# Performance work log

Measured on AMD Instinct MI355X. Metric: run time of the kernel, lower is better.

The kernel has to match this reference:

```python
import jax, jax.numpy as jnp
import numpy as np


def floor_ste(x):
    # forward: floor(x); backward: identity (straight-through estimator)
    return x + jax.lax.stop_gradient(jnp.floor(x) - x)


def _int_polynomial(x_int, sf):
    c0, c1, c2 = 0.35815147, 0.96963238, 1.0
    b_int = floor_ste((c1 / c0) / sf)
    c_int = floor_ste((c2 / c0) / (sf * sf))
    z = x_int * (x_int + b_int) + c_int
    return z, c0 * sf * sf


def _int_exp(x_int, sf):
    x0 = -0.69314718
    n = 15
    x0_int = floor_ste(x0 / sf)
    x_int = jnp.maximum(x_int, n * x0_int)
    q = floor_ste(x_int / x0_int)
    r = x_int - x0_int * q
    exp_int, exp_sf = _int_polynomial(r, sf)
    exp_int = jnp.maximum(floor_ste(exp_int * jnp.exp2(n - q)), 0.0)
    return exp_int, exp_sf / (2.0 ** n)


def _int_softmax(x, sf):
    x_int = x / sf
    x_int = x_int - jnp.max(x_int, axis=-1, keepdims=True)
    exp_int, exp_sf = _int_exp(x_int, sf)
    exp_int_sum = jnp.sum(exp_int, axis=-1, keepdims=True)
    return exp_int, exp_int_sum, exp_sf


def setup_inputs() -> dict:
    key = jax.random.key(0)
    k1, = jax.random.split(key, 1)
    x = jax.random.normal(k1, (2, 16, 1024, 1024), dtype=jnp.float32)
    scale = jnp.float32(0.05)          # activation quantization step
    threshold = jnp.array([0.1], dtype=jnp.float32)  # nn.Parameter init
    return {"x": x, "scale": scale, "threshold": threshold}


def reference(x, scale, threshold):
    output_bit = 8
    threshold_bits = 8
    exp_int, exp_int_sum, exp_sf = _int_softmax(x, scale)
    factor = floor_ste((2.0 ** 32) / exp_int_sum)
    out_scale_A = threshold / (2.0 ** output_bit - 1.0)   # shape [1]
    out_scale_B = 1.0 / (2.0 ** output_bit - 1.0)
    approx_threshold = (floor_ste(threshold * 2.0 ** threshold_bits)
                        * exp_int_sum / (2.0 ** threshold_bits))
    mask_A = exp_int <= approx_threshold
    exp_int_A = jnp.where(mask_A, exp_int, 0.0)
    exp_int_B = jnp.where(mask_A, 0.0, exp_int)
    softmax_int_A = floor_ste(exp_int_A * factor / ((2.0 ** 32) * out_scale_A))
    softmax_int_B = floor_ste(exp_int_B * factor / ((2.0 ** 32) * out_scale_B))
    softmax_int_B = jnp.minimum(softmax_int_B, 255.0)
    return softmax_int_A * out_scale_A + softmax_int_B * out_scale_B
```

## Files before the change

kernel.cpp:

```cpp
#include <hip/hip_runtime.h>
#include <math.h>

#pragma clang fp contract(off)

#define TPB 256
#define ROWLEN 1024

typedef float f32x4 __attribute__((ext_vector_type(4)));

__device__ __forceinline__ float wave_max_dpp(float m) {
    const int NEG_INF = 0xff800000;
    int v;
    v = __builtin_amdgcn_update_dpp(NEG_INF, __float_as_int(m), 0x111, 0xf, 0xf, false);
    m = fmaxf(m, __int_as_float(v));
    v = __builtin_amdgcn_update_dpp(NEG_INF, __float_as_int(m), 0x112, 0xf, 0xf, false);
    m = fmaxf(m, __int_as_float(v));
    v = __builtin_amdgcn_update_dpp(NEG_INF, __float_as_int(m), 0x114, 0xf, 0xf, false);
    m = fmaxf(m, __int_as_float(v));
    v = __builtin_amdgcn_update_dpp(NEG_INF, __float_as_int(m), 0x118, 0xf, 0xf, false);
    m = fmaxf(m, __int_as_float(v));
    v = __builtin_amdgcn_update_dpp(NEG_INF, __float_as_int(m), 0x142, 0xa, 0xf, false);
    m = fmaxf(m, __int_as_float(v));
    v = __builtin_amdgcn_update_dpp(NEG_INF, __float_as_int(m), 0x143, 0xc, 0xf, false);
    m = fmaxf(m, __int_as_float(v));
    return __int_as_float(__builtin_amdgcn_readlane(__float_as_int(m), 63));
}

__device__ __forceinline__ unsigned wave_sum_dpp_u32(unsigned a) {
    int v;
    v = __builtin_amdgcn_update_dpp(0, (int)a, 0x111, 0xf, 0xf, false); a += (unsigned)v;
    v = __builtin_amdgcn_update_dpp(0, (int)a, 0x112, 0xf, 0xf, false); a += (unsigned)v;
    v = __builtin_amdgcn_update_dpp(0, (int)a, 0x114, 0xf, 0xf, false); a += (unsigned)v;
    v = __builtin_amdgcn_update_dpp(0, (int)a, 0x118, 0xf, 0xf, false); a += (unsigned)v;
    v = __builtin_amdgcn_update_dpp(0, (int)a, 0x142, 0xa, 0xf, false); a += (unsigned)v;
    v = __builtin_amdgcn_update_dpp(0, (int)a, 0x143, 0xc, 0xf, false); a += (unsigned)v;
    return (unsigned)__builtin_amdgcn_readlane((int)a, 63);
}

__global__ __launch_bounds__(TPB) void qsplit_int_softmax_kernel(
    const float* __restrict__ x,
    const float* __restrict__ scale_p,
    const float* __restrict__ thr_p,
    float* __restrict__ out)
{
    const int tid  = threadIdx.x;
    const int lane = tid & 63;
    const int wid  = tid >> 6;
    const size_t base = (size_t)blockIdx.x * ROWLEN + (size_t)tid * 4;

    __shared__ float  smax[4];
    __shared__ double ssum[4];

    const float sf  = scale_p[0];
    const float thr = thr_p[0];

    const float rh = 1.0f / sf;
    const float er = __builtin_fmaf(-sf, rh, 1.0f);
    const float rl = rh * er;

    #define DF_DIV(a) ({ float _p = (a) * rh; \
                         float _e = __builtin_fmaf((a), rh, -_p); \
                         _p + __builtin_fmaf((a), rl, _e); })
    const float x0f    = floorf(DF_DIV(-0.69314718f));
    const float bfc    = floorf(DF_DIV(2.7073824f));
    const float s2     = sf * sf;
    const float r2h    = 1.0f / s2;
    const float r2e    = __builtin_fmaf(-s2, r2h, 1.0f);
    const float r2l    = r2h * r2e;
    const float cq     = __builtin_fmaf(2.7921141f, r2l,
                         2.7921141f * r2h);
    const float cfc    = floorf(cq);
    const float clampf = 15.0f * x0f;
    const float invx0f = 1.0f / x0f;

    const float osA  = thr / 255.0f;
    const float osB  = 1.0f / 255.0f;
    const float invA = 1.0f / (4294967296.0f * osA);
    const float invB = 1.0f / (4294967296.0f * osB);
    const float thrq = floorf(thr * 256.0f);

    const f32x4 xv = *(const f32x4*)(x + base);

    float xi[4];
    #pragma unroll
    for (int j = 0; j < 4; ++j) {
        const float xx = xv[j];
        const float p  = xx * rh;
        const float e  = __builtin_fmaf(xx, rh, -p);
        xi[j] = p + __builtin_fmaf(xx, rl, e);
    }

    float m = fmaxf(fmaxf(xi[0], xi[1]), fmaxf(xi[2], xi[3]));
    m = wave_max_dpp(m);
    if (lane == 0) smax[wid] = m;
    __syncthreads();
    m = fmaxf(fmaxf(smax[0], smax[1]), fmaxf(smax[2], smax[3]));

    float e4[4];
    unsigned usum = 0;
    #pragma unroll
    for (int j = 0; j < 4; ++j) {
        float v = xi[j] - m;
        v = fmaxf(v, clampf);
        const float qf = floorf(v * invx0f);
        const int   qi = (int)qf;
        const float r  = v - x0f * qf;
        const float t  = r + bfc;
        const float z  = r * t + cfc;
        float ei = floorf(ldexpf(z, 15 - qi));
        ei = fmaxf(ei, 0.0f);
        e4[j] = ei;
        usum += (unsigned)ei;
    }

    const unsigned lo = wave_sum_dpp_u32(usum & 0xFFFFu);
    const unsigned hi = wave_sum_dpp_u32(usum >> 16);
    if (lane == 0)
        ssum[wid] = (double)(((unsigned long long)hi << 16) + lo);
    __syncthreads();
    const double s = ((ssum[0] + ssum[1]) + ssum[2]) + ssum[3];

    const float fac_f = (float)floor(4294967296.0 / s);
    const float ath_f = (float)(((double)thrq * s) * (1.0 / 256.0));

    f32x4 o;
    #pragma unroll
    for (int j = 0; j < 4; ++j) {
        const float ei  = e4[j];
        const bool  isA = (ei <= ath_f);
        const float t1  = ei * fac_f;
        const float t2  = t1 * (isA ? invA : invB);
        float si = floorf(t2);
        si = fminf(si, isA ? 3.0e38f : 255.0f);
        o[j] = si * (isA ? osA : osB);
    }
    __builtin_nontemporal_store(o, (f32x4*)(out + base));
}

extern "C" void kernel_launch(void* const* d_in, const int* in_sizes, int n_in,
                              void* d_out, int out_size, void* d_ws, size_t ws_size,
                              hipStream_t stream) {
    const float* x     = (const float*)d_in[0];
    const float* scale = (const float*)d_in[1];
    const float* thr   = (const float*)d_in[2];
    float* out = (float*)d_out;

    const int total = in_sizes[0];
    const int rows  = total / ROWLEN;

    qsplit_int_softmax_kernel<<<dim3(rows), dim3(TPB), 0, stream>>>(
        x, scale, thr, out);
}
```

Measured before the change: 223.6 us.

## Use persistent grid-stride blocks with next-row prefetch in int softmax

```diff
diff --git a/kernel.cpp b/kernel.cpp
--- a/kernel.cpp
+++ b/kernel.cpp
@@ -5,6 +5,7 @@
 
 #define TPB 256
 #define ROWLEN 1024
+#define PERSIST_BLOCKS 2048
 
 typedef float f32x4 __attribute__((ext_vector_type(4)));
 
@@ -41,12 +42,12 @@
     const float* __restrict__ x,
     const float* __restrict__ scale_p,
     const float* __restrict__ thr_p,
-    float* __restrict__ out)
+    float* __restrict__ out,
+    const int rows)
 {
     const int tid  = threadIdx.x;
     const int lane = tid & 63;
     const int wid  = tid >> 6;
-    const size_t base = (size_t)blockIdx.x * ROWLEN + (size_t)tid * 4;
 
     __shared__ float  smax[4];
     __shared__ double ssum[4];
@@ -79,62 +80,78 @@
     const float invB = 1.0f / (4294967296.0f * osB);
     const float thrq = floorf(thr * 256.0f);
 
-    const f32x4 xv = *(const f32x4*)(x + base);
+    const int stride = gridDim.x;
+    int r = blockIdx.x;
+    if (r >= rows) return;
 
-    float xi[4];
-    #pragma unroll
-    for (int j = 0; j < 4; ++j) {
-        const float xx = xv[j];
-        const float p  = xx * rh;
-        const float e  = __builtin_fmaf(xx, rh, -p);
-        xi[j] = p + __builtin_fmaf(xx, rl, e);
+    f32x4 xv = *(const f32x4*)(x + (size_t)r * ROWLEN + (size_t)tid * 4);
+
+    for (;;) {
+        const int rn = r + stride;
+        const bool has_next = (rn < rows);
+        f32x4 xn;
+        if (has_next)
+            xn = *(const f32x4*)(x + (size_t)rn * ROWLEN + (size_t)tid * 4);
+
+        float xi[4];
+        #pragma unroll
+        for (int j = 0; j < 4; ++j) {
+            const float xx = xv[j];
+            const float p  = xx * rh;
+            const float e  = __builtin_fmaf(xx, rh, -p);
+            xi[j] = p + __builtin_fmaf(xx, rl, e);
+        }
+
+        float m = fmaxf(fmaxf(xi[0], xi[1]), fmaxf(xi[2], xi[3]));
+        m = wave_max_dpp(m);
+        if (lane == 0) smax[wid] = m;
+        __syncthreads();
+        m = fmaxf(fmaxf(smax[0], smax[1]), fmaxf(smax[2], smax[3]));
+
+        float e4[4];
+        unsigned usum = 0;
+        #pragma unroll
+        for (int j = 0; j < 4; ++j) {
+            float v = xi[j] - m;
+            v = fmaxf(v, clampf);
+            const float qf = floorf(v * invx0f);
+            const int   qi = (int)qf;
+            const float rr = v - x0f * qf;
+            const float t  = rr + bfc;
+            const float z  = rr * t + cfc;
+            float ei = floorf(ldexpf(z, 15 - qi));
+            ei = fmaxf(ei, 0.0f);
+            e4[j] = ei;
+            usum += (unsigned)ei;
+        }
+
+        const unsigned lo = wave_sum_dpp_u32(usum & 0xFFFFu);
+        const unsigned hi = wave_sum_dpp_u32(usum >> 16);
+        if (lane == 0)
+            ssum[wid] = (double)(((unsigned long long)hi << 16) + lo);
+        __syncthreads();
+        const double s = ((ssum[0] + ssum[1]) + ssum[2]) + ssum[3];
+
+        const float fac_f = (float)floor(4294967296.0 / s);
+        const float ath_f = (float)(((double)thrq * s) * (1.0 / 256.0));
+
+        f32x4 o;
+        #pragma unroll
+        for (int j = 0; j < 4; ++j) {
+            const float ei  = e4[j];
+            const bool  isA = (ei <= ath_f);
+            const float t1  = ei * fac_f;
+            const float t2  = t1 * (isA ? invA : invB);
+            float si = floorf(t2);
+            si = fminf(si, isA ? 3.0e38f : 255.0f);
+            o[j] = si * (isA ? osA : osB);
+        }
+        __builtin_nontemporal_store(o, (f32x4*)(out + (size_t)r * ROWLEN + (size_t)tid * 4));
+
+        if (!has_next) break;
+        r  = rn;
+        xv = xn;
     }
-
-    float m = fmaxf(fmaxf(xi[0], xi[1]), fmaxf(xi[2], xi[3]));
-    m = wave_max_dpp(m);
-    if (lane == 0) smax[wid] = m;
-    __syncthreads();
-    m = fmaxf(fmaxf(smax[0], smax[1]), fmaxf(smax[2], smax[3]));
-
-    float e4[4];
-    unsigned usum = 0;
-    #pragma unroll
-    for (int j = 0; j < 4; ++j) {
-        float v = xi[j] - m;
-        v = fmaxf(v, clampf);
-        const float qf = floorf(v * invx0f);
-        const int   qi = (int)qf;
-        const float r  = v - x0f * qf;
-        const float t  = r + bfc;
-        const float z  = r * t + cfc;
-        float ei = floorf(ldexpf(z, 15 - qi));
-        ei = fmaxf(ei, 0.0f);
-        e4[j] = ei;
-        usum += (unsigned)ei;
-    }
-
-    const unsigned lo = wave_sum_dpp_u32(usum & 0xFFFFu);
-    const unsigned hi = wave_sum_dpp_u32(usum >> 16);
-    if (lane == 0)
-        ssum[wid] = (double)(((unsigned long long)hi << 16) + lo);
-    __syncthreads();
-    const double s = ((ssum[0] + ssum[1]) + ssum[2]) + ssum[3];
-
-    const float fac_f = (float)floor(4294967296.0 / s);
-    const float ath_f = (float)(((double)thrq * s) * (1.0 / 256.0));
-
-    f32x4 o;
-    #pragma unroll
-    for (int j = 0; j < 4; ++j) {
-        const float ei  = e4[j];
-        const bool  isA = (ei <= ath_f);
-        const float t1  = ei * fac_f;
-        const float t2  = t1 * (isA ? invA : invB);
-        float si = floorf(t2);
-        si = fminf(si, isA ? 3.0e38f : 255.0f);
-        o[j] = si * (isA ? osA : osB);
-    }
-    __builtin_nontemporal_store(o, (f32x4*)(out + base));
 }
 
 extern "C" void kernel_launch(void* const* d_in, const int* in_sizes, int n_in,
@@ -148,6 +165,8 @@
     const int total = in_sizes[0];
     const int rows  = total / ROWLEN;
 
-    qsplit_int_softmax_kernel<<<dim3(rows), dim3(TPB), 0, stream>>>(
-        x, scale, thr, out);
+    const int blocks = rows < PERSIST_BLOCKS ? rows : PERSIST_BLOCKS;
+
+    qsplit_int_softmax_kernel<<<dim3(blocks), dim3(TPB), 0, stream>>>(
+        x, scale, thr, out, rows);
 }
```

Measured after the change: 235.2 us. 5.2% more time.
